# Optimization experiments

Hardware: AMD Instinct MI355X
Metric: run time of the kernel (lower is better)

## Reference

```python
import jax, jax.numpy as jnp
import numpy as np

# Config (Qwen3-4B-like, from ModelConfig defaults in source)
B = 32          # batch = number of decode requests = total_q
H = 32          # num_attention_heads
KVH = 8         # num_key_value_heads
G = H // KVH    # num_kv_groups = 4
D = 128         # head_dim
HID = 2560      # hidden_size
PS = 16         # page_size
MAXP = 128      # max_num_pages per request
NPAGES = B * MAXP   # 4096 pages in pool
MAXKV = MAXP * PS   # 2048
THETA = 5000000.0
EPS = 1e-6


def setup_inputs() -> dict:
    key = jax.random.key(0)
    ks = jax.random.split(key, 12)
    x = jax.random.normal(ks[0], (1, B, HID), dtype=jnp.float32)
    Wq = jax.random.normal(ks[1], (H * D, HID), dtype=jnp.float32) * 0.02
    Wk = jax.random.normal(ks[2], (KVH * D, HID), dtype=jnp.float32) * 0.02
    Wv = jax.random.normal(ks[3], (KVH * D, HID), dtype=jnp.float32) * 0.02
    Wo = jax.random.normal(ks[4], (HID, H * D), dtype=jnp.float32) * 0.02
    q_norm_w = jnp.ones((D,), dtype=jnp.float32)
    k_norm_w = jnp.ones((D,), dtype=jnp.float32)
    K_pool = jax.random.normal(ks[5], (NPAGES, PS, KVH, D), dtype=jnp.float32) * 0.02
    V_pool = jax.random.normal(ks[6], (NPAGES, PS, KVH, D), dtype=jnp.float32) * 0.02
    # each request owns a disjoint contiguous run of pages
    page_indices = jnp.arange(NPAGES, dtype=jnp.int32).reshape(B, MAXP)
    # KV length AFTER writing the single new decode token, in [128, MAXKV]
    lengths_after = jax.random.randint(ks[7], (B,), 128, MAXKV + 1).astype(jnp.int32)
    pos = lengths_after - 1                                  # position of new token
    page_of = page_indices[jnp.arange(B), pos // PS]         # page holding it
    slot_mapping = page_of.astype(jnp.int64) * PS + (pos % PS).astype(jnp.int64)
    # RoPE tables at the new-token positions: cos/sin (1, total_q, 1, D)
    inv_freq = 1.0 / (THETA ** (jnp.arange(0, D, 2, dtype=jnp.float32) / D))
    ang = pos.astype(jnp.float32)[:, None] * inv_freq[None, :]   # (B, D/2)
    ang = jnp.concatenate([ang, ang], axis=-1)                   # (B, D)
    cos = jnp.cos(ang)[None, :, None, :]
    sin = jnp.sin(ang)[None, :, None, :]
    return {"x": x, "cos": cos, "sin": sin, "Wq": Wq, "Wk": Wk, "Wv": Wv,
            "Wo": Wo, "q_norm_w": q_norm_w, "k_norm_w": k_norm_w,
            "K_pool": K_pool, "V_pool": V_pool, "page_indices": page_indices,
            "lengths_after": lengths_after, "slot_mapping": slot_mapping}


def _rmsnorm(x, w):
    xf = x.astype(jnp.float32)
    xf = xf * jax.lax.rsqrt(jnp.mean(xf * xf, axis=-1, keepdims=True) + EPS)
    return (w * xf).astype(x.dtype)


def _rope(x, cos, sin):
    # x: (1, heads, S, D); cos/sin: (1, S, 1, D) -> (1, 1, S, D)
    c = jnp.swapaxes(cos, 1, 2).astype(x.dtype)
    s = jnp.swapaxes(sin, 1, 2).astype(x.dtype)
    x1, x2 = jnp.split(x, 2, axis=-1)
    rot = jnp.concatenate([-x2, x1], axis=-1)
    return x * c + rot * s


def reference(x, cos, sin, Wq, Wk, Wv, Wo, q_norm_w, k_norm_w,
              K_pool, V_pool, page_indices, lengths_after, slot_mapping):
    total_q = x.shape[1]  # == B for decode
    # projections -> (1, heads, total_q, D)
    q = jnp.einsum('bsh,oh->bso', x, Wq).reshape(1, total_q, H, D).transpose(0, 2, 1, 3)
    k = jnp.einsum('bsh,oh->bso', x, Wk).reshape(1, total_q, KVH, D).transpose(0, 2, 1, 3)
    v = jnp.einsum('bsh,oh->bso', x, Wv).reshape(1, total_q, KVH, D).transpose(0, 2, 1, 3)
    # QK-norm (per-head RMSNorm on head_dim), then RoPE
    q = _rope(_rmsnorm(q, q_norm_w), cos, sin)
    k = _rope(_rmsnorm(k, k_norm_w), cos, sin)
    # write new K/V into the page pool (index_copy_ equivalent)
    k_pack = jnp.swapaxes(k[0], 0, 1)  # (total_q, KVH, D)
    v_pack = jnp.swapaxes(v[0], 0, 1)
    Kf = K_pool.reshape(NPAGES * PS, KVH, D).at[slot_mapping].set(k_pack)
    Vf = V_pool.reshape(NPAGES * PS, KVH, D).at[slot_mapping].set(v_pack)
    Kp = Kf.reshape(NPAGES, PS, KVH, D)
    Vp = Vf.reshape(NPAGES, PS, KVH, D)
    # decode path: full page-table gather per request
    flat_idx = page_indices.reshape(-1)
    k_all = Kp[flat_idx].reshape(B, MAXKV, KVH, D)
    v_all = Vp[flat_idx].reshape(B, MAXKV, KVH, D)
    # GQA attention, single query per request; scale = 1/sqrt(D) (SDPA default)
    qg = jnp.swapaxes(q[0], 0, 1).reshape(B, KVH, G, D)  # (B, KVH, G, D)
    scores = jnp.einsum('bkgd,bskd->bkgs', qg, k_all) * (1.0 / np.sqrt(D))
    invalid = jnp.arange(MAXKV)[None, :] >= lengths_after[:, None]  # (B, MAXKV)
    scores = jnp.where(invalid[:, None, None, :], -jnp.inf, scores)
    probs = jax.nn.softmax(scores, axis=-1)
    out = jnp.einsum('bkgs,bskd->bkgd', probs, v_all).reshape(B, H * D)
    y = jnp.einsum('bo,ho->bh', out, Wo)  # o_proj
    return y[None]  # (1, total_q, HID)
```

## Files before the change

kernel.cpp:

```cpp
#include <hip/hip_runtime.h>
#include <math.h>

#define NB    32
#define HIDV  2560
#define HD    128
#define NQH   32
#define NKVH  8

typedef __bf16 bf16x8 __attribute__((ext_vector_type(8)));
typedef float  f32x4  __attribute__((ext_vector_type(4)));

__device__ __forceinline__ unsigned bfpack(float a, float b) {
  unsigned ua = __float_as_uint(a), ub = __float_as_uint(b);
  ua = (ua + 0x7FFFu + ((ua >> 16) & 1u)) >> 16;
  ub = (ub + 0x7FFFu + ((ub >> 16) & 1u)) >> 16;
  return ua | (ub << 16);
}

__global__ __launch_bounds__(256) void gemm_part(
    const float* __restrict__ X, const float* __restrict__ W,
    float* __restrict__ P, int N, int K) {
  __shared__ __align__(16) unsigned short Wl[64 * 264];
  __shared__ __align__(16) unsigned short Xl[32 * 264];
  const int t  = threadIdx.x;
  const int f0 = blockIdx.x * 64;
  const int kc = blockIdx.y;

  const float* Wg = W + (size_t)f0 * K + (size_t)kc * 256;
  #pragma unroll
  for (int i = 0; i < 16; ++i) {
    int idx = i * 256 + t;
    int row = idx >> 6, c4 = idx & 63;
    float4 w4 = *(const float4*)(Wg + (size_t)row * K + c4 * 4);
    *(uint2*)((char*)Wl + row * 528 + c4 * 8) =
        make_uint2(bfpack(w4.x, w4.y), bfpack(w4.z, w4.w));
  }
  const float* Xg = X + (size_t)kc * 256;
  #pragma unroll
  for (int i = 0; i < 8; ++i) {
    int idx = i * 256 + t;
    int row = idx >> 6, c4 = idx & 63;
    float4 x4 = *(const float4*)(Xg + (size_t)row * K + c4 * 4);
    *(uint2*)((char*)Xl + row * 528 + c4 * 8) =
        make_uint2(bfpack(x4.x, x4.y), bfpack(x4.z, x4.w));
  }
  __syncthreads();

  const int w = t >> 6, l = t & 63;
  const int rA = l & 15, kq = l >> 4;
  f32x4 acc0 = {0.f, 0.f, 0.f, 0.f}, acc1 = {0.f, 0.f, 0.f, 0.f};
  const char* pa0 = (const char*)Xl + rA * 528 + kq * 16;
  const char* pa1 = pa0 + 16 * 528;
  const char* pb  = (const char*)Wl + (w * 16 + rA) * 528 + kq * 16;
  #pragma unroll
  for (int ks = 0; ks < 8; ++ks) {
    bf16x8 a0 = *(const bf16x8*)(pa0 + ks * 64);
    bf16x8 a1 = *(const bf16x8*)(pa1 + ks * 64);
    bf16x8 bb = *(const bf16x8*)(pb  + ks * 64);
    acc0 = __builtin_amdgcn_mfma_f32_16x16x32_bf16(a0, bb, acc0, 0, 0, 0);
    acc1 = __builtin_amdgcn_mfma_f32_16x16x32_bf16(a1, bb, acc1, 0, 0, 0);
  }
  const int fcol = f0 + w * 16 + rA;
  float* Pr = P + ((size_t)kc * 32) * N + fcol;
  #pragma unroll
  for (int j = 0; j < 4; ++j) {
    int b0 = kq * 4 + j;
    Pr[(size_t)b0 * N]        = acc0[j];
    Pr[(size_t)(b0 + 16) * N] = acc1[j];
  }
}

__global__ __launch_bounds__(128) void finqkv(
    const float* __restrict__ qp, const float* __restrict__ kp,
    const float* __restrict__ vp, const float* __restrict__ cosb,
    const float* __restrict__ sinb, const float* __restrict__ qw,
    const float* __restrict__ kw, float* __restrict__ qn,
    float* __restrict__ kn, float* __restrict__ vn) {
  const int b = blockIdx.x, h = blockIdx.y, d = threadIdx.x;
  float x = 0.f;
  if (h < 32) {
    #pragma unroll
    for (int c = 0; c < 10; ++c) x += qp[(size_t)(c * 32 + b) * 4096 + h * 128 + d];
  } else if (h < 40) {
    #pragma unroll
    for (int c = 0; c < 10; ++c) x += kp[(size_t)(c * 32 + b) * 1024 + (h - 32) * 128 + d];
  } else {
    #pragma unroll
    for (int c = 0; c < 10; ++c) x += vp[(size_t)(c * 32 + b) * 1024 + (h - 40) * 128 + d];
  }
  if (h >= 40) { vn[((size_t)b * 8 + (h - 40)) * 128 + d] = x; return; }

  __shared__ float red[2];
  __shared__ float sh[128];
  float ss = x * x;
  #pragma unroll
  for (int mk = 1; mk < 64; mk <<= 1) ss += __shfl_xor(ss, mk);
  if ((d & 63) == 0) red[d >> 6] = ss;
  __syncthreads();
  const float inv = rsqrtf((red[0] + red[1]) * (1.f / 128.f) + 1e-6f);
  const float* nw = (h < 32) ? qw : kw;
  const float xn = x * inv * nw[d];
  sh[d] = xn;
  __syncthreads();
  const float rot = (d < 64) ? -sh[d + 64] : sh[d - 64];
  const float o = xn * cosb[b * 128 + d] + rot * sinb[b * 128 + d];
  if (h < 32) qn[((size_t)b * 32 + h) * 128 + d] = o;
  else        kn[((size_t)b * 8 + (h - 32)) * 128 + d] = o;
}

__global__ __launch_bounds__(512) void attn(
    const float* __restrict__ Kp, const float* __restrict__ Vp,
    const float* __restrict__ qn, const float* __restrict__ kn,
    const float* __restrict__ vn, const int* __restrict__ pidx,
    const int* __restrict__ lens, float* __restrict__ ao) {
  const int b = blockIdx.x >> 3, kvh = blockIdx.x & 7;
  const int t = threadIdx.x, w = t >> 6, l = t & 63;
  const int sub = l >> 4, di = (l & 15) * 8;
  __shared__ int pages[128];
  __shared__ float mmS[32][4], msS[32][4];
  __shared__ __align__(16) float maccS[32][4][128];
  if (t < 128) pages[t] = pidx[b * 128 + t];
  __syncthreads();
  const int len = lens[b], lim = len - 1;

  float qf[4][8];
  const float SC = 0.08838834764831845f * 1.4426950408889634f;
  #pragma unroll
  for (int g = 0; g < 4; ++g)
    #pragma unroll
    for (int j = 0; j < 8; ++j)
      qf[g][j] = qn[((size_t)b * 32 + kvh * 4 + g) * 128 + di + j] * SC;

  float m[4], se[4], acc[4][8];
  #pragma unroll
  for (int g = 0; g < 4; ++g) {
    m[g] = -INFINITY; se[g] = 0.f;
    #pragma unroll
    for (int j = 0; j < 8; ++j) acc[g][j] = 0.f;
  }

  const int t0 = w * 4 + sub;
  const int nit = (lim + 31) >> 5;
  float4 k0, k1, v0, v1;
  {
    int tt = min(t0, lim - 1);
    size_t a = ((size_t)pages[tt >> 4] * 16 + (tt & 15)) * 1024 + kvh * 128 + di;
    k0 = *(const float4*)(Kp + a); k1 = *(const float4*)(Kp + a + 4);
    v0 = *(const float4*)(Vp + a); v1 = *(const float4*)(Vp + a + 4);
  }
  for (int it = 0; it < nit; ++it) {
    const float ck[8] = {k0.x, k0.y, k0.z, k0.w, k1.x, k1.y, k1.z, k1.w};
    const float cv[8] = {v0.x, v0.y, v0.z, v0.w, v1.x, v1.y, v1.z, v1.w};
    const int tc = t0 + it * 32;
    const bool valid = tc < lim;
    if (it + 1 < nit) {
      int tt = min(t0 + (it + 1) * 32, lim - 1);
      size_t a = ((size_t)pages[tt >> 4] * 16 + (tt & 15)) * 1024 + kvh * 128 + di;
      k0 = *(const float4*)(Kp + a); k1 = *(const float4*)(Kp + a + 4);
      v0 = *(const float4*)(Vp + a); v1 = *(const float4*)(Vp + a + 4);
    }
    float s[4];
    #pragma unroll
    for (int g = 0; g < 4; ++g) {
      float d8 = 0.f;
      #pragma unroll
      for (int j = 0; j < 8; ++j) d8 += qf[g][j] * ck[j];
      s[g] = d8;
    }
    #pragma unroll
    for (int mk = 1; mk < 16; mk <<= 1) {
      #pragma unroll
      for (int g = 0; g < 4; ++g) s[g] += __shfl_xor(s[g], mk);
    }
    if (valid) {
      #pragma unroll
      for (int g = 0; g < 4; ++g) {
        const float sg = s[g];
        if (sg > m[g]) {
          const float scf = exp2f(m[g] - sg);
          m[g] = sg;
          se[g] = se[g] * scf + 1.f;
          #pragma unroll
          for (int j = 0; j < 8; ++j) acc[g][j] = acc[g][j] * scf + cv[j];
        } else {
          const float p = exp2f(sg - m[g]);
          se[g] += p;
          #pragma unroll
          for (int j = 0; j < 8; ++j) acc[g][j] += p * cv[j];
        }
      }
    }
  }

  if (w == 0) {
    const float* kr = kn + ((size_t)b * 8 + kvh) * 128 + di;
    const float* vr = vn + ((size_t)b * 8 + kvh) * 128 + di;
    float ck[8], cv[8];
    #pragma unroll
    for (int j = 0; j < 8; ++j) { ck[j] = kr[j]; cv[j] = vr[j]; }
    float s[4];
    #pragma unroll
    for (int g = 0; g < 4; ++g) {
      float d8 = 0.f;
      #pragma unroll
      for (int j = 0; j < 8; ++j) d8 += qf[g][j] * ck[j];
      s[g] = d8;
    }
    #pragma unroll
    for (int mk = 1; mk < 16; mk <<= 1) {
      #pragma unroll
      for (int g = 0; g < 4; ++g) s[g] += __shfl_xor(s[g], mk);
    }
    if (sub == 0) {
      #pragma unroll
      for (int g = 0; g < 4; ++g) {
        const float sg = s[g];
        if (sg > m[g]) {
          const float scf = exp2f(m[g] - sg);
          m[g] = sg;
          se[g] = se[g] * scf + 1.f;
          #pragma unroll
          for (int j = 0; j < 8; ++j) acc[g][j] = acc[g][j] * scf + cv[j];
        } else {
          const float p = exp2f(sg - m[g]);
          se[g] += p;
          #pragma unroll
          for (int j = 0; j < 8; ++j) acc[g][j] += p * cv[j];
        }
      }
    }
  }

  const int st = w * 4 + sub;
  if ((l & 15) == 0) {
    #pragma unroll
    for (int g = 0; g < 4; ++g) { mmS[st][g] = m[g]; msS[st][g] = se[g]; }
  }
  #pragma unroll
  for (int g = 0; g < 4; ++g)
    #pragma unroll
    for (int j = 0; j < 8; ++j) maccS[st][g][di + j] = acc[g][j];
  __syncthreads();

  const int g = t >> 7, d = t & 127;
  float M = -INFINITY;
  #pragma unroll
  for (int s2 = 0; s2 < 32; ++s2) M = fmaxf(M, mmS[s2][g]);
  float den = 0.f, num = 0.f;
  for (int s2 = 0; s2 < 32; ++s2) {
    const float wg = exp2f(mmS[s2][g] - M);
    den += wg * msS[s2][g];
    num += wg * maccS[s2][g][d];
  }
  ao[((size_t)b * 32 + kvh * 4 + g) * 128 + d] = num / den;
}

__global__ __launch_bounds__(256) void oreduce(const float* __restrict__ op,
                                               float* __restrict__ y) {
  const int i = blockIdx.x * 256 + threadIdx.x;
  float s = 0.f;
  #pragma unroll
  for (int c = 0; c < 16; ++c) s += op[(size_t)c * (32 * 2560) + i];
  y[i] = s;
}

extern "C" void kernel_launch(void* const* d_in, const int* in_sizes, int n_in,
                              void* d_out, int out_size, void* d_ws, size_t ws_size,
                              hipStream_t stream) {
  const float* x    = (const float*)d_in[0];
  const float* cosb = (const float*)d_in[1];
  const float* sinb = (const float*)d_in[2];
  const float* Wq   = (const float*)d_in[3];
  const float* Wk   = (const float*)d_in[4];
  const float* Wv   = (const float*)d_in[5];
  const float* Wo   = (const float*)d_in[6];
  const float* qw   = (const float*)d_in[7];
  const float* kw   = (const float*)d_in[8];
  const float* Kp   = (const float*)d_in[9];
  const float* Vp   = (const float*)d_in[10];
  const int*   pidx = (const int*)d_in[11];
  const int*   lens = (const int*)d_in[12];
  float* y = (float*)d_out;

  float* ws = (float*)d_ws;
  float* qp = ws;
  float* kp = qp + 1310720;
  float* vp = kp + 327680;
  float* qn = vp + 327680;
  float* kn = qn + 131072;
  float* vn = kn + 32768;
  float* ao = vn + 32768;
  float* op = qp;
  (void)in_sizes; (void)n_in; (void)out_size; (void)ws_size;

  gemm_part<<<dim3(64, 10), 256, 0, stream>>>(x, Wq, qp, 4096, 2560);
  gemm_part<<<dim3(16, 10), 256, 0, stream>>>(x, Wk, kp, 1024, 2560);
  gemm_part<<<dim3(16, 10), 256, 0, stream>>>(x, Wv, vp, 1024, 2560);
  finqkv<<<dim3(32, 48), 128, 0, stream>>>(qp, kp, vp, cosb, sinb, qw, kw, qn, kn, vn);
  attn<<<256, 512, 0, stream>>>(Kp, Vp, qn, kn, vn, pidx, lens, ao);
  gemm_part<<<dim3(40, 16), 256, 0, stream>>>(ao, Wo, op, 2560, 4096);
  oreduce<<<320, 256, 0, stream>>>(op, y);
}
```

Baseline: 105.2 us.

## Split decode attention across KV chunks and fuse QKV GEMM launches

Attention is split into up to 8 chunks of 256 tokens per (batch, kv-head), each handled by a 256-thread block that writes partial max, denominator and accumulator to workspace. A separate merge kernel then combines the chunks, flash-decoding style. This raises the number of blocks from 256 to up to 2048 so the CUs are better occupied and long sequences no longer dominate the critical path. The three QKV projection GEMMs are also merged into a single launch. The cost is an extra kernel launch and a round trip of partial results through global memory.

```diff
diff --git a/kernel.cpp b/kernel.cpp
--- a/kernel.cpp
+++ b/kernel.cpp
@@ -6,6 +6,7 @@
 #define HD    128
 #define NQH   32
 #define NKVH  8
+#define CHUNK 256
 
 typedef __bf16 bf16x8 __attribute__((ext_vector_type(8)));
 typedef float  f32x4  __attribute__((ext_vector_type(4)));
@@ -17,15 +18,10 @@
   return ua | (ub << 16);
 }
 
-__global__ __launch_bounds__(256) void gemm_part(
+__device__ __forceinline__ void gemm_body(
     const float* __restrict__ X, const float* __restrict__ W,
-    float* __restrict__ P, int N, int K) {
-  __shared__ __align__(16) unsigned short Wl[64 * 264];
-  __shared__ __align__(16) unsigned short Xl[32 * 264];
-  const int t  = threadIdx.x;
-  const int f0 = blockIdx.x * 64;
-  const int kc = blockIdx.y;
-
+    float* __restrict__ P, int N, int K, int f0, int kc, int t,
+    unsigned short* Wl, unsigned short* Xl) {
   const float* Wg = W + (size_t)f0 * K + (size_t)kc * 256;
   #pragma unroll
   for (int i = 0; i < 16; ++i) {
@@ -68,6 +64,28 @@
     Pr[(size_t)b0 * N]        = acc0[j];
     Pr[(size_t)(b0 + 16) * N] = acc1[j];
   }
+}
+
+__global__ __launch_bounds__(256) void qkv_gemm(
+    const float* __restrict__ X, const float* __restrict__ Wq,
+    const float* __restrict__ Wk, const float* __restrict__ Wv,
+    float* __restrict__ qp, float* __restrict__ kp, float* __restrict__ vp) {
+  __shared__ __align__(16) unsigned short Wl[64 * 264];
+  __shared__ __align__(16) unsigned short Xl[32 * 264];
+  const int bx = blockIdx.x;
+  const float* W; float* P; int N, f0;
+  if (bx < 64)      { W = Wq; P = qp; N = 4096; f0 = bx * 64; }
+  else if (bx < 80) { W = Wk; P = kp; N = 1024; f0 = (bx - 64) * 64; }
+  else              { W = Wv; P = vp; N = 1024; f0 = (bx - 80) * 64; }
+  gemm_body(X, W, P, N, 2560, f0, blockIdx.y, threadIdx.x, Wl, Xl);
+}
+
+__global__ __launch_bounds__(256) void o_gemm(
+    const float* __restrict__ X, const float* __restrict__ W,
+    float* __restrict__ P) {
+  __shared__ __align__(16) unsigned short Wl[64 * 264];
+  __shared__ __align__(16) unsigned short Xl[32 * 264];
+  gemm_body(X, W, P, 2560, 4096, blockIdx.x * 64, blockIdx.y, threadIdx.x, Wl, Xl);
 }
 
 __global__ __launch_bounds__(128) void finqkv(
@@ -108,20 +126,26 @@
   else        kn[((size_t)b * 8 + (h - 32)) * 128 + d] = o;
 }
 
-__global__ __launch_bounds__(512) void attn(
+__global__ __launch_bounds__(256) void attn_chunk(
     const float* __restrict__ Kp, const float* __restrict__ Vp,
     const float* __restrict__ qn, const float* __restrict__ kn,
     const float* __restrict__ vn, const int* __restrict__ pidx,
-    const int* __restrict__ lens, float* __restrict__ ao) {
-  const int b = blockIdx.x >> 3, kvh = blockIdx.x & 7;
+    const int* __restrict__ lens, float* __restrict__ pm,
+    float* __restrict__ pse, float* __restrict__ pacc) {
+  const int c = blockIdx.x, bk = blockIdx.y;
+  const int b = bk >> 3, kvh = bk & 7;
+  const int len = lens[b], lim = len - 1;
+  const int base = c * CHUNK;
+  if (c > 0 && base >= lim) return;
+  const int cnt = min(CHUNK, lim - base);
+
   const int t = threadIdx.x, w = t >> 6, l = t & 63;
-  const int sub = l >> 4, di = (l & 15) * 8;
-  __shared__ int pages[128];
-  __shared__ float mmS[32][4], msS[32][4];
-  __shared__ __align__(16) float maccS[32][4][128];
-  if (t < 128) pages[t] = pidx[b * 128 + t];
-  __syncthreads();
-  const int len = lens[b], lim = len - 1;
+  const int sub = l >> 4, st = w * 4 + sub, di = (l & 15) * 8;
+  __shared__ int pages[16];
+  __shared__ float mmS[16][4], msS[16][4];
+  __shared__ __align__(16) float maccS[16][4][128];
+  if (t < 16) pages[t] = pidx[b * 128 + c * 16 + t];
+  __syncthreads();
 
   float qf[4][8];
   const float SC = 0.08838834764831845f * 1.4426950408889634f;
@@ -139,23 +163,21 @@
     for (int j = 0; j < 8; ++j) acc[g][j] = 0.f;
   }
 
-  const int t0 = w * 4 + sub;
-  const int nit = (lim + 31) >> 5;
+  const int nit = (cnt + 15) >> 4;
   float4 k0, k1, v0, v1;
   {
-    int tt = min(t0, lim - 1);
-    size_t a = ((size_t)pages[tt >> 4] * 16 + (tt & 15)) * 1024 + kvh * 128 + di;
+    int tt = base + min(st, cnt - 1);
+    size_t a = ((size_t)pages[(tt >> 4) - c * 16] * 16 + (tt & 15)) * 1024 + kvh * 128 + di;
     k0 = *(const float4*)(Kp + a); k1 = *(const float4*)(Kp + a + 4);
     v0 = *(const float4*)(Vp + a); v1 = *(const float4*)(Vp + a + 4);
   }
   for (int it = 0; it < nit; ++it) {
     const float ck[8] = {k0.x, k0.y, k0.z, k0.w, k1.x, k1.y, k1.z, k1.w};
     const float cv[8] = {v0.x, v0.y, v0.z, v0.w, v1.x, v1.y, v1.z, v1.w};
-    const int tc = t0 + it * 32;
-    const bool valid = tc < lim;
+    const bool valid = it * 16 + st < cnt;
     if (it + 1 < nit) {
-      int tt = min(t0 + (it + 1) * 32, lim - 1);
-      size_t a = ((size_t)pages[tt >> 4] * 16 + (tt & 15)) * 1024 + kvh * 128 + di;
+      int tt = base + min((it + 1) * 16 + st, cnt - 1);
+      size_t a = ((size_t)pages[(tt >> 4) - c * 16] * 16 + (tt & 15)) * 1024 + kvh * 128 + di;
       k0 = *(const float4*)(Kp + a); k1 = *(const float4*)(Kp + a + 4);
       v0 = *(const float4*)(Vp + a); v1 = *(const float4*)(Vp + a + 4);
     }
@@ -192,7 +214,7 @@
     }
   }
 
-  if (w == 0) {
+  if (c == 0 && w == 0) {
     const float* kr = kn + ((size_t)b * 8 + kvh) * 128 + di;
     const float* vr = vn + ((size_t)b * 8 + kvh) * 128 + di;
     float ck[8], cv[8];
@@ -231,7 +253,6 @@
     }
   }
 
-  const int st = w * 4 + sub;
   if ((l & 15) == 0) {
     #pragma unroll
     for (int g = 0; g < 4; ++g) { mmS[st][g] = m[g]; msS[st][g] = se[g]; }
@@ -242,15 +263,39 @@
     for (int j = 0; j < 8; ++j) maccS[st][g][di + j] = acc[g][j];
   __syncthreads();
 
-  const int g = t >> 7, d = t & 127;
+  #pragma unroll
+  for (int r = 0; r < 2; ++r) {
+    const int idx = r * 256 + t, g = idx >> 7, d = idx & 127;
+    float M = -INFINITY;
+    #pragma unroll
+    for (int s2 = 0; s2 < 16; ++s2) M = fmaxf(M, mmS[s2][g]);
+    float den = 0.f, num = 0.f;
+    #pragma unroll
+    for (int s2 = 0; s2 < 16; ++s2) {
+      const float wg = exp2f(mmS[s2][g] - M);
+      den += wg * msS[s2][g];
+      num += wg * maccS[s2][g][d];
+    }
+    if (d == 0) { pm[(bk * 8 + c) * 4 + g] = M; pse[(bk * 8 + c) * 4 + g] = den; }
+    pacc[((size_t)(bk * 8 + c) * 4 + g) * 128 + d] = num;
+  }
+}
+
+__global__ __launch_bounds__(512) void attn_merge(
+    const float* __restrict__ pm, const float* __restrict__ pse,
+    const float* __restrict__ pacc, const int* __restrict__ lens,
+    float* __restrict__ ao) {
+  const int bk = blockIdx.x, b = bk >> 3, kvh = bk & 7;
+  const int t = threadIdx.x, g = t >> 7, d = t & 127;
+  const int lim = lens[b] - 1;
+  const int nch = max(1, (lim + CHUNK - 1) / CHUNK);
   float M = -INFINITY;
-  #pragma unroll
-  for (int s2 = 0; s2 < 32; ++s2) M = fmaxf(M, mmS[s2][g]);
+  for (int c = 0; c < nch; ++c) M = fmaxf(M, pm[(bk * 8 + c) * 4 + g]);
   float den = 0.f, num = 0.f;
-  for (int s2 = 0; s2 < 32; ++s2) {
-    const float wg = exp2f(mmS[s2][g] - M);
-    den += wg * msS[s2][g];
-    num += wg * maccS[s2][g][d];
+  for (int c = 0; c < nch; ++c) {
+    const float wg = exp2f(pm[(bk * 8 + c) * 4 + g] - M);
+    den += wg * pse[(bk * 8 + c) * 4 + g];
+    num += wg * pacc[((size_t)(bk * 8 + c) * 4 + g) * 128 + d];
   }
   ao[((size_t)b * 32 + kvh * 4 + g) * 128 + d] = num / den;
 }
@@ -290,14 +335,16 @@
   float* kn = qn + 131072;
   float* vn = kn + 32768;
   float* ao = vn + 32768;
+  float* pm = ao + 131072;
+  float* pse = pm + 8192;
+  float* pacc = pse + 8192;
   float* op = qp;
   (void)in_sizes; (void)n_in; (void)out_size; (void)ws_size;
 
-  gemm_part<<<dim3(64, 10), 256, 0, stream>>>(x, Wq, qp, 4096, 2560);
-  gemm_part<<<dim3(16, 10), 256, 0, stream>>>(x, Wk, kp, 1024, 2560);
-  gemm_part<<<dim3(16, 10), 256, 0, stream>>>(x, Wv, vp, 1024, 2560);
+  qkv_gemm<<<dim3(96, 10), 256, 0, stream>>>(x, Wq, Wk, Wv, qp, kp, vp);
   finqkv<<<dim3(32, 48), 128, 0, stream>>>(qp, kp, vp, cosb, sinb, qw, kw, qn, kn, vn);
-  attn<<<256, 512, 0, stream>>>(Kp, Vp, qn, kn, vn, pidx, lens, ao);
-  gemm_part<<<dim3(40, 16), 256, 0, stream>>>(ao, Wo, op, 2560, 4096);
+  attn_chunk<<<dim3(8, 256), 256, 0, stream>>>(Kp, Vp, qn, kn, vn, pidx, lens, pm, pse, pacc);
+  attn_merge<<<256, 512, 0, stream>>>(pm, pse, pacc, lens, ao);
+  o_gemm<<<dim3(40, 16), 256, 0, stream>>>(ao, Wo, op);
   oreduce<<<320, 256, 0, stream>>>(op, y);
 }
```

New measurement: 114.6 us. 1.09x slower.

## Fuse QKV GEMMs, fold norm/RoPE into attention, halve split-K, use nontemporal loads

Applied to the files above, without the earlier changes.

Merges the three QKV projection launches into one kernel and has each GEMM block process two K slabs, which halves the split-K partials. The partial reduction, RMSNorm and RoPE move from the separate finqkv kernel into the start of the attention kernel, which stages the results in shared memory. Weight and KV-pool loads switch to nontemporal loads. This removes two launches and the qn/kn/vn round trips, but the GEMM grids are smaller and attention blocks redo some reduction work.

```diff
diff --git a/kernel.cpp b/kernel.cpp
--- a/kernel.cpp
+++ b/kernel.cpp
@@ -17,51 +17,55 @@
   return ua | (ub << 16);
 }
 
-__global__ __launch_bounds__(256) void gemm_part(
+__device__ __forceinline__ f32x4 nt_load4(const float* p) {
+  return __builtin_nontemporal_load((const f32x4*)p);
+}
+
+__device__ __forceinline__ void gemm_body(
     const float* __restrict__ X, const float* __restrict__ W,
-    float* __restrict__ P, int N, int K) {
-  __shared__ __align__(16) unsigned short Wl[64 * 264];
-  __shared__ __align__(16) unsigned short Xl[32 * 264];
-  const int t  = threadIdx.x;
-  const int f0 = blockIdx.x * 64;
-  const int kc = blockIdx.y;
-
-  const float* Wg = W + (size_t)f0 * K + (size_t)kc * 256;
-  #pragma unroll
-  for (int i = 0; i < 16; ++i) {
-    int idx = i * 256 + t;
-    int row = idx >> 6, c4 = idx & 63;
-    float4 w4 = *(const float4*)(Wg + (size_t)row * K + c4 * 4);
-    *(uint2*)((char*)Wl + row * 528 + c4 * 8) =
-        make_uint2(bfpack(w4.x, w4.y), bfpack(w4.z, w4.w));
-  }
-  const float* Xg = X + (size_t)kc * 256;
-  #pragma unroll
-  for (int i = 0; i < 8; ++i) {
-    int idx = i * 256 + t;
-    int row = idx >> 6, c4 = idx & 63;
-    float4 x4 = *(const float4*)(Xg + (size_t)row * K + c4 * 4);
-    *(uint2*)((char*)Xl + row * 528 + c4 * 8) =
-        make_uint2(bfpack(x4.x, x4.y), bfpack(x4.z, x4.w));
-  }
-  __syncthreads();
-
+    float* __restrict__ P, int N, int K, int f0, int kc0, int slabs, int t,
+    unsigned short* Wl, unsigned short* Xl) {
   const int w = t >> 6, l = t & 63;
   const int rA = l & 15, kq = l >> 4;
   f32x4 acc0 = {0.f, 0.f, 0.f, 0.f}, acc1 = {0.f, 0.f, 0.f, 0.f};
-  const char* pa0 = (const char*)Xl + rA * 528 + kq * 16;
-  const char* pa1 = pa0 + 16 * 528;
-  const char* pb  = (const char*)Wl + (w * 16 + rA) * 528 + kq * 16;
-  #pragma unroll
-  for (int ks = 0; ks < 8; ++ks) {
-    bf16x8 a0 = *(const bf16x8*)(pa0 + ks * 64);
-    bf16x8 a1 = *(const bf16x8*)(pa1 + ks * 64);
-    bf16x8 bb = *(const bf16x8*)(pb  + ks * 64);
-    acc0 = __builtin_amdgcn_mfma_f32_16x16x32_bf16(a0, bb, acc0, 0, 0, 0);
-    acc1 = __builtin_amdgcn_mfma_f32_16x16x32_bf16(a1, bb, acc1, 0, 0, 0);
+
+  for (int s = 0; s < slabs; ++s) {
+    const int kc = kc0 * slabs + s;
+    if (s) __syncthreads();
+    const float* Wg = W + (size_t)f0 * K + (size_t)kc * 256;
+    #pragma unroll
+    for (int i = 0; i < 16; ++i) {
+      int idx = i * 256 + t;
+      int row = idx >> 6, c4 = idx & 63;
+      f32x4 w4 = nt_load4(Wg + (size_t)row * K + c4 * 4);
+      *(uint2*)((char*)Wl + row * 528 + c4 * 8) =
+          make_uint2(bfpack(w4.x, w4.y), bfpack(w4.z, w4.w));
+    }
+    const float* Xg = X + (size_t)kc * 256;
+    #pragma unroll
+    for (int i = 0; i < 8; ++i) {
+      int idx = i * 256 + t;
+      int row = idx >> 6, c4 = idx & 63;
+      float4 x4 = *(const float4*)(Xg + (size_t)row * K + c4 * 4);
+      *(uint2*)((char*)Xl + row * 528 + c4 * 8) =
+          make_uint2(bfpack(x4.x, x4.y), bfpack(x4.z, x4.w));
+    }
+    __syncthreads();
+
+    const char* pa0 = (const char*)Xl + rA * 528 + kq * 16;
+    const char* pa1 = pa0 + 16 * 528;
+    const char* pb  = (const char*)Wl + (w * 16 + rA) * 528 + kq * 16;
+    #pragma unroll
+    for (int ks = 0; ks < 8; ++ks) {
+      bf16x8 a0 = *(const bf16x8*)(pa0 + ks * 64);
+      bf16x8 a1 = *(const bf16x8*)(pa1 + ks * 64);
+      bf16x8 bb = *(const bf16x8*)(pb  + ks * 64);
+      acc0 = __builtin_amdgcn_mfma_f32_16x16x32_bf16(a0, bb, acc0, 0, 0, 0);
+      acc1 = __builtin_amdgcn_mfma_f32_16x16x32_bf16(a1, bb, acc1, 0, 0, 0);
+    }
   }
   const int fcol = f0 + w * 16 + rA;
-  float* Pr = P + ((size_t)kc * 32) * N + fcol;
+  float* Pr = P + ((size_t)kc0 * 32) * N + fcol;
   #pragma unroll
   for (int j = 0; j < 4; ++j) {
     int b0 = kq * 4 + j;
@@ -70,48 +74,34 @@
   }
 }
 
-__global__ __launch_bounds__(128) void finqkv(
+__global__ __launch_bounds__(256) void qkv_gemm(
+    const float* __restrict__ X, const float* __restrict__ Wq,
+    const float* __restrict__ Wk, const float* __restrict__ Wv,
+    float* __restrict__ qp, float* __restrict__ kp, float* __restrict__ vp) {
+  __shared__ __align__(16) unsigned short Wl[64 * 264];
+  __shared__ __align__(16) unsigned short Xl[32 * 264];
+  const int bx = blockIdx.x;
+  const float* W; float* P; int N, f0;
+  if (bx < 64)      { W = Wq; P = qp; N = 4096; f0 = bx * 64; }
+  else if (bx < 80) { W = Wk; P = kp; N = 1024; f0 = (bx - 64) * 64; }
+  else              { W = Wv; P = vp; N = 1024; f0 = (bx - 80) * 64; }
+  gemm_body(X, W, P, N, 2560, f0, blockIdx.y, 2, threadIdx.x, Wl, Xl);
+}
+
+__global__ __launch_bounds__(256) void o_gemm(
+    const float* __restrict__ X, const float* __restrict__ W,
+    float* __restrict__ P) {
+  __shared__ __align__(16) unsigned short Wl[64 * 264];
+  __shared__ __align__(16) unsigned short Xl[32 * 264];
+  gemm_body(X, W, P, 2560, 4096, blockIdx.x * 64, blockIdx.y, 2, threadIdx.x, Wl, Xl);
+}
+
+__global__ __launch_bounds__(512) void attn(
+    const float* __restrict__ Kp, const float* __restrict__ Vp,
     const float* __restrict__ qp, const float* __restrict__ kp,
     const float* __restrict__ vp, const float* __restrict__ cosb,
     const float* __restrict__ sinb, const float* __restrict__ qw,
-    const float* __restrict__ kw, float* __restrict__ qn,
-    float* __restrict__ kn, float* __restrict__ vn) {
-  const int b = blockIdx.x, h = blockIdx.y, d = threadIdx.x;
-  float x = 0.f;
-  if (h < 32) {
-    #pragma unroll
-    for (int c = 0; c < 10; ++c) x += qp[(size_t)(c * 32 + b) * 4096 + h * 128 + d];
-  } else if (h < 40) {
-    #pragma unroll
-    for (int c = 0; c < 10; ++c) x += kp[(size_t)(c * 32 + b) * 1024 + (h - 32) * 128 + d];
-  } else {
-    #pragma unroll
-    for (int c = 0; c < 10; ++c) x += vp[(size_t)(c * 32 + b) * 1024 + (h - 40) * 128 + d];
-  }
-  if (h >= 40) { vn[((size_t)b * 8 + (h - 40)) * 128 + d] = x; return; }
-
-  __shared__ float red[2];
-  __shared__ float sh[128];
-  float ss = x * x;
-  #pragma unroll
-  for (int mk = 1; mk < 64; mk <<= 1) ss += __shfl_xor(ss, mk);
-  if ((d & 63) == 0) red[d >> 6] = ss;
-  __syncthreads();
-  const float inv = rsqrtf((red[0] + red[1]) * (1.f / 128.f) + 1e-6f);
-  const float* nw = (h < 32) ? qw : kw;
-  const float xn = x * inv * nw[d];
-  sh[d] = xn;
-  __syncthreads();
-  const float rot = (d < 64) ? -sh[d + 64] : sh[d - 64];
-  const float o = xn * cosb[b * 128 + d] + rot * sinb[b * 128 + d];
-  if (h < 32) qn[((size_t)b * 32 + h) * 128 + d] = o;
-  else        kn[((size_t)b * 8 + (h - 32)) * 128 + d] = o;
-}
-
-__global__ __launch_bounds__(512) void attn(
-    const float* __restrict__ Kp, const float* __restrict__ Vp,
-    const float* __restrict__ qn, const float* __restrict__ kn,
-    const float* __restrict__ vn, const int* __restrict__ pidx,
+    const float* __restrict__ kw, const int* __restrict__ pidx,
     const int* __restrict__ lens, float* __restrict__ ao) {
   const int b = blockIdx.x >> 3, kvh = blockIdx.x & 7;
   const int t = threadIdx.x, w = t >> 6, l = t & 63;
@@ -119,17 +109,67 @@
   __shared__ int pages[128];
   __shared__ float mmS[32][4], msS[32][4];
   __shared__ __align__(16) float maccS[32][4][128];
+  float* qlds = &maccS[0][0][0];
+  float* klds = qlds + 512;
+  float* vlds = klds + 128;
+  float* rsum = vlds + 128;
+
   if (t < 128) pages[t] = pidx[b * 128 + t];
-  __syncthreads();
+
+  const int role = t >> 7, d = t & 127;
+  float xq = 0.f;
+  #pragma unroll
+  for (int c = 0; c < 5; ++c)
+    xq += qp[((size_t)c * 32 + b) * 4096 + (kvh * 4 + role) * 128 + d];
+  float xk = 0.f, xv = 0.f;
+  if (t < 128) {
+    #pragma unroll
+    for (int c = 0; c < 5; ++c)
+      xk += kp[((size_t)c * 32 + b) * 1024 + kvh * 128 + d];
+  } else if (t < 256) {
+    #pragma unroll
+    for (int c = 0; c < 5; ++c)
+      xv += vp[((size_t)c * 32 + b) * 1024 + kvh * 128 + d];
+  }
+  float ssq = xq * xq;
+  #pragma unroll
+  for (int mk = 1; mk < 64; mk <<= 1) ssq += __shfl_xor(ssq, mk);
+  if (l == 0) rsum[w] = ssq;
+  if (t < 128) {
+    float ssk = xk * xk;
+    #pragma unroll
+    for (int mk = 1; mk < 64; mk <<= 1) ssk += __shfl_xor(ssk, mk);
+    if (l == 0) rsum[8 + w] = ssk;
+  }
+  __syncthreads();
+  const float cb = cosb[b * 128 + d], sb = sinb[b * 128 + d];
+  const float invq = rsqrtf((rsum[role * 2] + rsum[role * 2 + 1]) * (1.f / 128.f) + 1e-6f);
+  const float xnq = xq * invq * qw[d];
+  qlds[role * 128 + d] = xnq;
+  float xnk = 0.f;
+  if (t < 128) {
+    const float invk = rsqrtf((rsum[8] + rsum[9]) * (1.f / 128.f) + 1e-6f);
+    xnk = xk * invk * kw[d];
+    klds[d] = xnk;
+  } else if (t < 256) {
+    vlds[d] = xv;
+  }
+  __syncthreads();
+  const float rpq = qlds[role * 128 + (d ^ 64)];
+  const float rpk = (t < 128) ? klds[d ^ 64] : 0.f;
+  __syncthreads();
+  qlds[role * 128 + d] = xnq * cb + ((d < 64) ? -rpq : rpq) * sb;
+  if (t < 128) klds[d] = xnk * cb + ((d < 64) ? -rpk : rpk) * sb;
+  __syncthreads();
+
   const int len = lens[b], lim = len - 1;
-
   float qf[4][8];
   const float SC = 0.08838834764831845f * 1.4426950408889634f;
   #pragma unroll
   for (int g = 0; g < 4; ++g)
     #pragma unroll
     for (int j = 0; j < 8; ++j)
-      qf[g][j] = qn[((size_t)b * 32 + kvh * 4 + g) * 128 + di + j] * SC;
+      qf[g][j] = qlds[g * 128 + di + j] * SC;
 
   float m[4], se[4], acc[4][8];
   #pragma unroll
@@ -141,23 +181,22 @@
 
   const int t0 = w * 4 + sub;
   const int nit = (lim + 31) >> 5;
-  float4 k0, k1, v0, v1;
+  f32x4 k0, k1, v0, v1;
   {
     int tt = min(t0, lim - 1);
     size_t a = ((size_t)pages[tt >> 4] * 16 + (tt & 15)) * 1024 + kvh * 128 + di;
-    k0 = *(const float4*)(Kp + a); k1 = *(const float4*)(Kp + a + 4);
-    v0 = *(const float4*)(Vp + a); v1 = *(const float4*)(Vp + a + 4);
+    k0 = nt_load4(Kp + a); k1 = nt_load4(Kp + a + 4);
+    v0 = nt_load4(Vp + a); v1 = nt_load4(Vp + a + 4);
   }
   for (int it = 0; it < nit; ++it) {
-    const float ck[8] = {k0.x, k0.y, k0.z, k0.w, k1.x, k1.y, k1.z, k1.w};
-    const float cv[8] = {v0.x, v0.y, v0.z, v0.w, v1.x, v1.y, v1.z, v1.w};
-    const int tc = t0 + it * 32;
-    const bool valid = tc < lim;
+    const float ck[8] = {k0[0], k0[1], k0[2], k0[3], k1[0], k1[1], k1[2], k1[3]};
+    const float cv[8] = {v0[0], v0[1], v0[2], v0[3], v1[0], v1[1], v1[2], v1[3]};
+    const bool valid = it * 32 + t0 < lim;
     if (it + 1 < nit) {
-      int tt = min(t0 + (it + 1) * 32, lim - 1);
+      int tt = min((it + 1) * 32 + t0, lim - 1);
       size_t a = ((size_t)pages[tt >> 4] * 16 + (tt & 15)) * 1024 + kvh * 128 + di;
-      k0 = *(const float4*)(Kp + a); k1 = *(const float4*)(Kp + a + 4);
-      v0 = *(const float4*)(Vp + a); v1 = *(const float4*)(Vp + a + 4);
+      k0 = nt_load4(Kp + a); k1 = nt_load4(Kp + a + 4);
+      v0 = nt_load4(Vp + a); v1 = nt_load4(Vp + a + 4);
     }
     float s[4];
     #pragma unroll
@@ -193,11 +232,9 @@
   }
 
   if (w == 0) {
-    const float* kr = kn + ((size_t)b * 8 + kvh) * 128 + di;
-    const float* vr = vn + ((size_t)b * 8 + kvh) * 128 + di;
     float ck[8], cv[8];
     #pragma unroll
-    for (int j = 0; j < 8; ++j) { ck[j] = kr[j]; cv[j] = vr[j]; }
+    for (int j = 0; j < 8; ++j) { ck[j] = klds[di + j]; cv[j] = vlds[di + j]; }
     float s[4];
     #pragma unroll
     for (int g = 0; g < 4; ++g) {
@@ -242,7 +279,7 @@
     for (int j = 0; j < 8; ++j) maccS[st][g][di + j] = acc[g][j];
   __syncthreads();
 
-  const int g = t >> 7, d = t & 127;
+  const int g = t >> 7, dd = t & 127;
   float M = -INFINITY;
   #pragma unroll
   for (int s2 = 0; s2 < 32; ++s2) M = fmaxf(M, mmS[s2][g]);
@@ -250,9 +287,9 @@
   for (int s2 = 0; s2 < 32; ++s2) {
     const float wg = exp2f(mmS[s2][g] - M);
     den += wg * msS[s2][g];
-    num += wg * maccS[s2][g][d];
-  }
-  ao[((size_t)b * 32 + kvh * 4 + g) * 128 + d] = num / den;
+    num += wg * maccS[s2][g][dd];
+  }
+  ao[((size_t)b * 32 + kvh * 4 + g) * 128 + dd] = num / den;
 }
 
 __global__ __launch_bounds__(256) void oreduce(const float* __restrict__ op,
@@ -260,7 +297,7 @@
   const int i = blockIdx.x * 256 + threadIdx.x;
   float s = 0.f;
   #pragma unroll
-  for (int c = 0; c < 16; ++c) s += op[(size_t)c * (32 * 2560) + i];
+  for (int c = 0; c < 8; ++c) s += op[(size_t)c * (32 * 2560) + i];
   y[i] = s;
 }
 
@@ -284,20 +321,14 @@
 
   float* ws = (float*)d_ws;
   float* qp = ws;
-  float* kp = qp + 1310720;
-  float* vp = kp + 327680;
-  float* qn = vp + 327680;
-  float* kn = qn + 131072;
-  float* vn = kn + 32768;
-  float* ao = vn + 32768;
+  float* kp = qp + 655360;
+  float* vp = kp + 163840;
+  float* ao = vp + 163840;
   float* op = qp;
   (void)in_sizes; (void)n_in; (void)out_size; (void)ws_size;
 
-  gemm_part<<<dim3(64, 10), 256, 0, stream>>>(x, Wq, qp, 4096, 2560);
-  gemm_part<<<dim3(16, 10), 256, 0, stream>>>(x, Wk, kp, 1024, 2560);
-  gemm_part<<<dim3(16, 10), 256, 0, stream>>>(x, Wv, vp, 1024, 2560);
-  finqkv<<<dim3(32, 48), 128, 0, stream>>>(qp, kp, vp, cosb, sinb, qw, kw, qn, kn, vn);
-  attn<<<256, 512, 0, stream>>>(Kp, Vp, qn, kn, vn, pidx, lens, ao);
-  gemm_part<<<dim3(40, 16), 256, 0, stream>>>(ao, Wo, op, 2560, 4096);
+  qkv_gemm<<<dim3(96, 5), 256, 0, stream>>>(x, Wq, Wk, Wv, qp, kp, vp);
+  attn<<<256, 512, 0, stream>>>(Kp, Vp, qp, kp, vp, cosb, sinb, qw, kw, pidx, lens, ao);
+  o_gemm<<<dim3(40, 8), 256, 0, stream>>>(ao, Wo, op);
   oreduce<<<320, 256, 0, stream>>>(op, y);
 }
```

Result: slower. 111.6 us (+6.1%).

## Merge QKV GEMM launches and double-buffer KV prefetch in attention

Applied to the files above, without the earlier changes.

The three separate Q/K/V projection launches are merged into one grid of 96x10 blocks that dispatches by block index, removing two launches and letting all projection blocks share the GPU at once. The attention loop now keeps two outstanding register prefetch buffers (two tokens ahead) instead of one, to hide more global memory latency on the paged KV gather. The O projection gets a specialised kernel with constant sizes. The deeper prefetch raises register use per thread, which may lower occupancy.

```diff
diff --git a/kernel.cpp b/kernel.cpp
--- a/kernel.cpp
+++ b/kernel.cpp
@@ -17,15 +17,10 @@
   return ua | (ub << 16);
 }
 
-__global__ __launch_bounds__(256) void gemm_part(
+__device__ __forceinline__ void gemm_body(
     const float* __restrict__ X, const float* __restrict__ W,
-    float* __restrict__ P, int N, int K) {
-  __shared__ __align__(16) unsigned short Wl[64 * 264];
-  __shared__ __align__(16) unsigned short Xl[32 * 264];
-  const int t  = threadIdx.x;
-  const int f0 = blockIdx.x * 64;
-  const int kc = blockIdx.y;
-
+    float* __restrict__ P, int N, int K, int f0, int kc, int t,
+    unsigned short* Wl, unsigned short* Xl) {
   const float* Wg = W + (size_t)f0 * K + (size_t)kc * 256;
   #pragma unroll
   for (int i = 0; i < 16; ++i) {
@@ -68,6 +63,28 @@
     Pr[(size_t)b0 * N]        = acc0[j];
     Pr[(size_t)(b0 + 16) * N] = acc1[j];
   }
+}
+
+__global__ __launch_bounds__(256) void qkv_gemm(
+    const float* __restrict__ X, const float* __restrict__ Wq,
+    const float* __restrict__ Wk, const float* __restrict__ Wv,
+    float* __restrict__ qp, float* __restrict__ kp, float* __restrict__ vp) {
+  __shared__ __align__(16) unsigned short Wl[64 * 264];
+  __shared__ __align__(16) unsigned short Xl[32 * 264];
+  const int bx = blockIdx.x;
+  const float* W; float* P; int N, f0;
+  if (bx < 64)      { W = Wq; P = qp; N = 4096; f0 = bx * 64; }
+  else if (bx < 80) { W = Wk; P = kp; N = 1024; f0 = (bx - 64) * 64; }
+  else              { W = Wv; P = vp; N = 1024; f0 = (bx - 80) * 64; }
+  gemm_body(X, W, P, N, 2560, f0, blockIdx.y, threadIdx.x, Wl, Xl);
+}
+
+__global__ __launch_bounds__(256) void o_gemm(
+    const float* __restrict__ X, const float* __restrict__ W,
+    float* __restrict__ P) {
+  __shared__ __align__(16) unsigned short Wl[64 * 264];
+  __shared__ __align__(16) unsigned short Xl[32 * 264];
+  gemm_body(X, W, P, 2560, 4096, blockIdx.x * 64, blockIdx.y, threadIdx.x, Wl, Xl);
 }
 
 __global__ __launch_bounds__(128) void finqkv(
@@ -141,24 +158,8 @@
 
   const int t0 = w * 4 + sub;
   const int nit = (lim + 31) >> 5;
-  float4 k0, k1, v0, v1;
-  {
-    int tt = min(t0, lim - 1);
-    size_t a = ((size_t)pages[tt >> 4] * 16 + (tt & 15)) * 1024 + kvh * 128 + di;
-    k0 = *(const float4*)(Kp + a); k1 = *(const float4*)(Kp + a + 4);
-    v0 = *(const float4*)(Vp + a); v1 = *(const float4*)(Vp + a + 4);
-  }
-  for (int it = 0; it < nit; ++it) {
-    const float ck[8] = {k0.x, k0.y, k0.z, k0.w, k1.x, k1.y, k1.z, k1.w};
-    const float cv[8] = {v0.x, v0.y, v0.z, v0.w, v1.x, v1.y, v1.z, v1.w};
-    const int tc = t0 + it * 32;
-    const bool valid = tc < lim;
-    if (it + 1 < nit) {
-      int tt = min(t0 + (it + 1) * 32, lim - 1);
-      size_t a = ((size_t)pages[tt >> 4] * 16 + (tt & 15)) * 1024 + kvh * 128 + di;
-      k0 = *(const float4*)(Kp + a); k1 = *(const float4*)(Kp + a + 4);
-      v0 = *(const float4*)(Vp + a); v1 = *(const float4*)(Vp + a + 4);
-    }
+
+  auto update = [&](const float (&ck)[8], const float (&cv)[8], bool valid) {
     float s[4];
     #pragma unroll
     for (int g = 0; g < 4; ++g) {
@@ -190,6 +191,44 @@
         }
       }
     }
+  };
+
+  f32x4 ka0, ka1, va0, va1, kb0, kb1, vb0, vb1;
+  {
+    int tt = min(t0, lim - 1);
+    size_t a = ((size_t)pages[tt >> 4] * 16 + (tt & 15)) * 1024 + kvh * 128 + di;
+    ka0 = *(const f32x4*)(Kp + a); ka1 = *(const f32x4*)(Kp + a + 4);
+    va0 = *(const f32x4*)(Vp + a); va1 = *(const f32x4*)(Vp + a + 4);
+  }
+  if (nit > 1) {
+    int tt = min(32 + t0, lim - 1);
+    size_t a = ((size_t)pages[tt >> 4] * 16 + (tt & 15)) * 1024 + kvh * 128 + di;
+    kb0 = *(const f32x4*)(Kp + a); kb1 = *(const f32x4*)(Kp + a + 4);
+    vb0 = *(const f32x4*)(Vp + a); vb1 = *(const f32x4*)(Vp + a + 4);
+  }
+  for (int it = 0; it < nit; it += 2) {
+    {
+      const float ck[8] = {ka0[0], ka0[1], ka0[2], ka0[3], ka1[0], ka1[1], ka1[2], ka1[3]};
+      const float cv[8] = {va0[0], va0[1], va0[2], va0[3], va1[0], va1[1], va1[2], va1[3]};
+      if (it + 2 < nit) {
+        int tt = min((it + 2) * 32 + t0, lim - 1);
+        size_t a = ((size_t)pages[tt >> 4] * 16 + (tt & 15)) * 1024 + kvh * 128 + di;
+        ka0 = *(const f32x4*)(Kp + a); ka1 = *(const f32x4*)(Kp + a + 4);
+        va0 = *(const f32x4*)(Vp + a); va1 = *(const f32x4*)(Vp + a + 4);
+      }
+      update(ck, cv, it * 32 + t0 < lim);
+    }
+    if (it + 1 < nit) {
+      const float ck[8] = {kb0[0], kb0[1], kb0[2], kb0[3], kb1[0], kb1[1], kb1[2], kb1[3]};
+      const float cv[8] = {vb0[0], vb0[1], vb0[2], vb0[3], vb1[0], vb1[1], vb1[2], vb1[3]};
+      if (it + 3 < nit) {
+        int tt = min((it + 3) * 32 + t0, lim - 1);
+        size_t a = ((size_t)pages[tt >> 4] * 16 + (tt & 15)) * 1024 + kvh * 128 + di;
+        kb0 = *(const f32x4*)(Kp + a); kb1 = *(const f32x4*)(Kp + a + 4);
+        vb0 = *(const f32x4*)(Vp + a); vb1 = *(const f32x4*)(Vp + a + 4);
+      }
+      update(ck, cv, (it + 1) * 32 + t0 < lim);
+    }
   }
 
   if (w == 0) {
@@ -198,37 +237,7 @@
     float ck[8], cv[8];
     #pragma unroll
     for (int j = 0; j < 8; ++j) { ck[j] = kr[j]; cv[j] = vr[j]; }
-    float s[4];
-    #pragma unroll
-    for (int g = 0; g < 4; ++g) {
-      float d8 = 0.f;
-      #pragma unroll
-      for (int j = 0; j < 8; ++j) d8 += qf[g][j] * ck[j];
-      s[g] = d8;
-    }
-    #pragma unroll
-    for (int mk = 1; mk < 16; mk <<= 1) {
-      #pragma unroll
-      for (int g = 0; g < 4; ++g) s[g] += __shfl_xor(s[g], mk);
-    }
-    if (sub == 0) {
-      #pragma unroll
-      for (int g = 0; g < 4; ++g) {
-        const float sg = s[g];
-        if (sg > m[g]) {
-          const float scf = exp2f(m[g] - sg);
-          m[g] = sg;
-          se[g] = se[g] * scf + 1.f;
-          #pragma unroll
-          for (int j = 0; j < 8; ++j) acc[g][j] = acc[g][j] * scf + cv[j];
-        } else {
-          const float p = exp2f(sg - m[g]);
-          se[g] += p;
-          #pragma unroll
-          for (int j = 0; j < 8; ++j) acc[g][j] += p * cv[j];
-        }
-      }
-    }
+    update(ck, cv, sub == 0);
   }
 
   const int st = w * 4 + sub;
@@ -242,7 +251,7 @@
     for (int j = 0; j < 8; ++j) maccS[st][g][di + j] = acc[g][j];
   __syncthreads();
 
-  const int g = t >> 7, d = t & 127;
+  const int g = t >> 7, dd = t & 127;
   float M = -INFINITY;
   #pragma unroll
   for (int s2 = 0; s2 < 32; ++s2) M = fmaxf(M, mmS[s2][g]);
@@ -250,9 +259,9 @@
   for (int s2 = 0; s2 < 32; ++s2) {
     const float wg = exp2f(mmS[s2][g] - M);
     den += wg * msS[s2][g];
-    num += wg * maccS[s2][g][d];
-  }
-  ao[((size_t)b * 32 + kvh * 4 + g) * 128 + d] = num / den;
+    num += wg * maccS[s2][g][dd];
+  }
+  ao[((size_t)b * 32 + kvh * 4 + g) * 128 + dd] = num / den;
 }
 
 __global__ __launch_bounds__(256) void oreduce(const float* __restrict__ op,
@@ -293,11 +302,9 @@
   float* op = qp;
   (void)in_sizes; (void)n_in; (void)out_size; (void)ws_size;
 
-  gemm_part<<<dim3(64, 10), 256, 0, stream>>>(x, Wq, qp, 4096, 2560);
-  gemm_part<<<dim3(16, 10), 256, 0, stream>>>(x, Wk, kp, 1024, 2560);
-  gemm_part<<<dim3(16, 10), 256, 0, stream>>>(x, Wv, vp, 1024, 2560);
+  qkv_gemm<<<dim3(96, 10), 256, 0, stream>>>(x, Wq, Wk, Wv, qp, kp, vp);
   finqkv<<<dim3(32, 48), 128, 0, stream>>>(qp, kp, vp, cosb, sinb, qw, kw, qn, kn, vn);
   attn<<<256, 512, 0, stream>>>(Kp, Vp, qn, kn, vn, pidx, lens, ao);
-  gemm_part<<<dim3(40, 16), 256, 0, stream>>>(ao, Wo, op, 2560, 4096);
+  o_gemm<<<dim3(40, 16), 256, 0, stream>>>(ao, Wo, op);
   oreduce<<<320, 256, 0, stream>>>(op, y);
 }
```

After: 99.00 us. 1.06x faster.
